# Performance work log

Hardware: AMD Instinct MI355X
Metric: run time of the kernel (lower is better)

The kernel has to match this reference:

```python
import jax, jax.numpy as jnp
import numpy as np

NUM_BINS = 4
NUM_CELLS = NUM_BINS ** 3


def _generate_grids(num_bins):
    # cell-center coordinates in the unit cube, matching generate_grids()
    c = (jnp.arange(num_bins, dtype=jnp.float32) + 1.0) / num_bins - 0.5 / num_bins
    gx, gy, gz = jnp.meshgrid(c, c, c, indexing='ij')
    return jnp.stack([gx.ravel(), gy.ravel(), gz.ravel()], axis=1)  # [C, 3]


def setup_inputs() -> dict:
    key = jax.random.key(0)
    x = jax.random.normal(key, (64, 65536, 6), dtype=jnp.float32)
    return {"input": x}


def reference(input):
    B, P, _ = input.shape
    pos = input[..., 0:3]
    ori = input[..., 3:6]

    # symmetric bounding cube: bbox_max over points and xyz dims
    bbox_max = jnp.max(jnp.abs(pos), axis=(1, 2), keepdims=True)          # [B,1,1]
    thickness = jnp.clip(2.0 * bbox_max, 1e-5, None)
    pos_in_cube = (pos + bbox_max) / thickness                            # [B,P,3] in [0,1]

    ci = jnp.clip((pos_in_cube * NUM_BINS).astype(jnp.int32), 0, NUM_BINS - 1)
    cell_idx = (ci[..., 0] * NUM_BINS + ci[..., 1]) * NUM_BINS + ci[..., 2]  # [B,P]

    seg = lambda vals, idx: jax.ops.segment_sum(vals, idx, num_segments=NUM_CELLS)

    # per-cell point counts
    freq = jax.vmap(seg)(jnp.ones((B, P), jnp.float32), cell_idx)[..., None]  # [B,C,1]
    freq_c = jnp.clip(freq, 1.0, None)
    uprefix = 1.0 / jnp.sqrt(freq_c)
    f_freq = 0.001 * freq * uprefix                                       # [B,C,1]

    # mean offset from cell centers
    grids = _generate_grids(NUM_BINS)                                     # [C,3]
    offsets = pos_in_cube - grids[cell_idx]                               # [B,P,3]
    f_mean = jax.vmap(seg)(offsets, cell_idx) * uprefix                   # [B,C,3]

    # upper-triangular orientation covariance: xx,xy,xz,yy,yz,zz
    ox, oy, oz = ori[..., 0], ori[..., 1], ori[..., 2]
    cov = jnp.stack([ox * ox, ox * oy, ox * oz, oy * oy, oy * oz, oz * oz], axis=-1)  # [B,P,6]
    f_normcov = jax.vmap(seg)(cov, cell_idx) / freq_c                     # [B,C,6]

    f_all = jnp.concatenate([f_freq, f_mean, f_normcov], axis=2).reshape(B, -1)  # [B, C*10]
    norm = jnp.linalg.norm(f_all, axis=1, keepdims=True)
    return f_all / jnp.clip(norm, 1e-12, None)
```

## Files before the change

kernel.cpp:

```cpp
#include <hip/hip_runtime.h>


#define BATCH 64
#define NPTS 65536
#define FEAT 640
#define COPIES 16
#define CSTRIDE 16
#define S_OFF 262144.0f
#define S_COV 4096.0f

__device__ __forceinline__ void bin_point(int* h, int k,
                                          float px, float py, float pz,
                                          float ox, float oy, float oz,
                                          float bmax, float inv_thick) {
    float sx = (px + bmax) * inv_thick;
    float sy = (py + bmax) * inv_thick;
    float sz = (pz + bmax) * inv_thick;
    int cx = (int)(sx * 4.0f); cx = cx < 0 ? 0 : (cx > 3 ? 3 : cx);
    int cy = (int)(sy * 4.0f); cy = cy < 0 ? 0 : (cy > 3 ? 3 : cy);
    int cz = (int)(sz * 4.0f); cz = cz < 0 ? 0 : (cz > 3 ? 3 : cz);
    int cell = (cx * 4 + cy) * 4 + cz;
    float offx = sx - (cx * 0.25f + 0.125f);
    float offy = sy - (cy * 0.25f + 0.125f);
    float offz = sz - (cz * 0.25f + 0.125f);
    int kk = k ^ (cell & 15);
    int a = cell * (10 * CSTRIDE) + kk;
    atomicAdd(&h[a + 0 * CSTRIDE], 1);
    atomicAdd(&h[a + 1 * CSTRIDE], __float2int_rn(offx * S_OFF));
    atomicAdd(&h[a + 2 * CSTRIDE], __float2int_rn(offy * S_OFF));
    atomicAdd(&h[a + 3 * CSTRIDE], __float2int_rn(offz * S_OFF));
    atomicAdd(&h[a + 4 * CSTRIDE], __float2int_rn(ox * ox * S_COV));
    atomicAdd(&h[a + 5 * CSTRIDE], __float2int_rn(ox * oy * S_COV));
    atomicAdd(&h[a + 6 * CSTRIDE], __float2int_rn(ox * oz * S_COV));
    atomicAdd(&h[a + 7 * CSTRIDE], __float2int_rn(oy * oy * S_COV));
    atomicAdd(&h[a + 8 * CSTRIDE], __float2int_rn(oy * oz * S_COV));
    atomicAdd(&h[a + 9 * CSTRIDE], __float2int_rn(oz * oz * S_COV));
}

__global__ __launch_bounds__(256) void k_bbox(const float* __restrict__ x,
                                              unsigned int* __restrict__ part,
                                              unsigned long long* __restrict__ acc) {
    int b = blockIdx.y;
    int fb = b * 16 + blockIdx.x;
    if (threadIdx.x < 40) acc[fb * 40 + threadIdx.x] = 0ULL;

    const float4* F = (const float4*)(x + (size_t)b * NPTS * 6);
    int tid = blockIdx.x * 256 + threadIdx.x;
    int tm = tid % 3;
    float m = 0.0f;
    #pragma unroll
    for (int o = 0; o < 2; ++o) {
        #pragma unroll
        for (int u = 0; u < 12; ++u) {
            int it = o * 12 + u;
            float4 v = F[tid + it * 4096];
            int mm = tm + (u % 3);
            mm = mm >= 3 ? mm - 3 : mm;
            float ax = fabsf(v.x), ay = fabsf(v.y), az = fabsf(v.z), aw = fabsf(v.w);
            float c0 = fmaxf(fmaxf(ax, ay), az);
            float c1 = fmaxf(az, aw);
            float cand = mm == 0 ? c0 : (mm == 1 ? c1 : ax);
            m = fmaxf(m, cand);
        }
    }
    for (int off = 32; off > 0; off >>= 1) m = fmaxf(m, __shfl_down(m, off, 64));
    __shared__ float s[4];
    if ((threadIdx.x & 63) == 0) s[threadIdx.x >> 6] = m;
    __syncthreads();
    if (threadIdx.x == 0) {
        m = fmaxf(fmaxf(s[0], s[1]), fmaxf(s[2], s[3]));
        part[fb] = __float_as_uint(m);
    }
}

__global__ __launch_bounds__(256) void k_bin(const float* __restrict__ x,
                                             const unsigned int* __restrict__ part,
                                             unsigned long long* __restrict__ acc) {
    __shared__ int h[FEAT * CSTRIDE];
    for (int i = threadIdx.x; i < FEAT * CSTRIDE; i += 256) h[i] = 0;
    int b = blockIdx.y;
    unsigned int um = 0u;
    #pragma unroll
    for (int p = 0; p < 16; ++p) um = um > part[b * 16 + p] ? um : part[b * 16 + p];
    float bmax = __uint_as_float(um);
    float thick = fmaxf(2.0f * bmax, 1e-5f);
    float inv_thick = 1.0f / thick;
    __syncthreads();

    const float4* base = (const float4*)(x + (size_t)b * NPTS * 6);
    int tid = blockIdx.x * 256 + threadIdx.x;
    int k = threadIdx.x & (COPIES - 1);
    #pragma unroll
    for (int it = 0; it < 8; ++it) {
        int i = tid + it * 4096;
        float4 f0 = base[3 * i + 0];
        float4 f1 = base[3 * i + 1];
        float4 f2 = base[3 * i + 2];
        bin_point(h, k, f0.x, f0.y, f0.z, f0.w, f1.x, f1.y, bmax, inv_thick);
        bin_point(h, k, f1.z, f1.w, f2.x, f2.y, f2.z, f2.w, bmax, inv_thick);
    }
    __syncthreads();
    for (int v = threadIdx.x; v < FEAT; v += 256) {
        long long sum = 0;
        #pragma unroll
        for (int c = 0; c < COPIES; ++c) sum += (long long)h[v * CSTRIDE + c];
        atomicAdd(&acc[b * FEAT + v], (unsigned long long)sum);
    }
}

__global__ __launch_bounds__(640) void k_final(const unsigned long long* __restrict__ acc,
                                               float* __restrict__ out) {
    int b = blockIdx.x;
    int t = threadIdx.x;
    int cell = t / 10, j = t - cell * 10;
    long long ni = (long long)acc[b * FEAT + cell * 10];
    long long vi = (long long)acc[b * FEAT + t];
    float n = (float)ni;
    float fc = fmaxf(n, 1.0f);
    float up = 1.0f / sqrtf(fc);
    float val;
    if (j == 0)      val = 0.001f * n * up;
    else if (j < 4)  val = ((float)vi * (1.0f / S_OFF)) * up;
    else             val = ((float)vi * (1.0f / S_COV)) / fc;

    __shared__ float red[12];
    float s = val * val;
    for (int off = 32; off > 0; off >>= 1) s += __shfl_down(s, off, 64);
    if ((t & 63) == 0) red[t >> 6] = s;
    __syncthreads();
    if (t == 0) {
        float tot = 0.0f;
        #pragma unroll
        for (int w = 0; w < 10; ++w) tot += red[w];
        red[10] = fmaxf(sqrtf(tot), 1e-12f);
    }
    __syncthreads();
    out[b * FEAT + t] = val / red[10];
}

extern "C" void kernel_launch(void* const* d_in, const int* in_sizes, int n_in,
                              void* d_out, int out_size, void* d_ws, size_t ws_size,
                              hipStream_t stream) {
    const float* x = (const float*)d_in[0];
    float* out = (float*)d_out;
    unsigned int* part = (unsigned int*)d_ws;
    unsigned long long* acc = (unsigned long long*)((char*)d_ws + 4096);

    dim3 grid(16, BATCH);
    k_bbox<<<grid, 256, 0, stream>>>(x, part, acc);
    k_bin<<<grid, 256, 0, stream>>>(x, part, acc);
    k_final<<<BATCH, 640, 0, stream>>>(acc, out);
}
```

Before: 162.2 us.

## Pack pairs of biased 32-bit accumulators into 64-bit LDS atomics

Replaces ten 32-bit shared-memory atomics per point with five 64-bit atomics, each packing two quantized feature values. Each value is biased to stay non-negative so the low half never borrows from the high half, and the bias is subtracted after reduction using the per-cell count. This halves the number of LDS atomic operations in the binning hot loop. In exchange the 64-bit atomics may be slower per operation, the cell/copy layout changes bank-conflict behaviour, and the 32-bit halves can overflow if a cell receives enough points, since each biased value can approach 2^19.

```diff
diff --git a/kernel.cpp b/kernel.cpp
--- a/kernel.cpp
+++ b/kernel.cpp
@@ -5,11 +5,12 @@
 #define NPTS 65536
 #define FEAT 640
 #define COPIES 16
-#define CSTRIDE 16
 #define S_OFF 262144.0f
 #define S_COV 4096.0f
+#define BIAS  262144
 
-__device__ __forceinline__ void bin_point(int* h, int k,
+
+__device__ __forceinline__ void bin_point(unsigned long long* h, int k,
                                           float px, float py, float pz,
                                           float ox, float oy, float oz,
                                           float bmax, float inv_thick) {
@@ -23,18 +24,22 @@
     float offx = sx - (cx * 0.25f + 0.125f);
     float offy = sy - (cy * 0.25f + 0.125f);
     float offz = sz - (cz * 0.25f + 0.125f);
+    int qx = __float2int_rn(offx * S_OFF) + BIAS;
+    int qy = __float2int_rn(offy * S_OFF) + BIAS;
+    int qz = __float2int_rn(offz * S_OFF) + BIAS;
+    int c0 = __float2int_rn(ox * ox * S_COV) + BIAS;
+    int c1 = __float2int_rn(ox * oy * S_COV) + BIAS;
+    int c2 = __float2int_rn(ox * oz * S_COV) + BIAS;
+    int c3 = __float2int_rn(oy * oy * S_COV) + BIAS;
+    int c4 = __float2int_rn(oy * oz * S_COV) + BIAS;
+    int c5 = __float2int_rn(oz * oz * S_COV) + BIAS;
     int kk = k ^ (cell & 15);
-    int a = cell * (10 * CSTRIDE) + kk;
-    atomicAdd(&h[a + 0 * CSTRIDE], 1);
-    atomicAdd(&h[a + 1 * CSTRIDE], __float2int_rn(offx * S_OFF));
-    atomicAdd(&h[a + 2 * CSTRIDE], __float2int_rn(offy * S_OFF));
-    atomicAdd(&h[a + 3 * CSTRIDE], __float2int_rn(offz * S_OFF));
-    atomicAdd(&h[a + 4 * CSTRIDE], __float2int_rn(ox * ox * S_COV));
-    atomicAdd(&h[a + 5 * CSTRIDE], __float2int_rn(ox * oy * S_COV));
-    atomicAdd(&h[a + 6 * CSTRIDE], __float2int_rn(ox * oz * S_COV));
-    atomicAdd(&h[a + 7 * CSTRIDE], __float2int_rn(oy * oy * S_COV));
-    atomicAdd(&h[a + 8 * CSTRIDE], __float2int_rn(oy * oz * S_COV));
-    atomicAdd(&h[a + 9 * CSTRIDE], __float2int_rn(oz * oz * S_COV));
+    unsigned long long* p = h + (size_t)cell * (5 * COPIES) + kk;
+    atomicAdd(p + 0 * COPIES, ((unsigned long long)(unsigned)qx << 32) | 1ULL);
+    atomicAdd(p + 1 * COPIES, ((unsigned long long)(unsigned)qz << 32) | (unsigned)qy);
+    atomicAdd(p + 2 * COPIES, ((unsigned long long)(unsigned)c1 << 32) | (unsigned)c0);
+    atomicAdd(p + 3 * COPIES, ((unsigned long long)(unsigned)c3 << 32) | (unsigned)c2);
+    atomicAdd(p + 4 * COPIES, ((unsigned long long)(unsigned)c5 << 32) | (unsigned)c4);
 }
 
 __global__ __launch_bounds__(256) void k_bbox(const float* __restrict__ x,
@@ -76,8 +81,8 @@
 __global__ __launch_bounds__(256) void k_bin(const float* __restrict__ x,
                                              const unsigned int* __restrict__ part,
                                              unsigned long long* __restrict__ acc) {
-    __shared__ int h[FEAT * CSTRIDE];
-    for (int i = threadIdx.x; i < FEAT * CSTRIDE; i += 256) h[i] = 0;
+    __shared__ unsigned long long h[64 * 5 * COPIES];
+    for (int i = threadIdx.x; i < 64 * 5 * COPIES; i += 256) h[i] = 0ULL;
     int b = blockIdx.y;
     unsigned int um = 0u;
     #pragma unroll
@@ -100,11 +105,34 @@
         bin_point(h, k, f1.z, f1.w, f2.x, f2.y, f2.z, f2.w, bmax, inv_thick);
     }
     __syncthreads();
-    for (int v = threadIdx.x; v < FEAT; v += 256) {
-        long long sum = 0;
+
+    for (int cell = threadIdx.x; cell < 64; cell += 256) {
+        unsigned long long s = 0ULL;
         #pragma unroll
-        for (int c = 0; c < COPIES; ++c) sum += (long long)h[v * CSTRIDE + c];
-        atomicAdd(&acc[b * FEAT + v], (unsigned long long)sum);
+        for (int c = 0; c < COPIES; ++c) s += h[(cell * 5 + 0) * COPIES + c];
+        h[cell * 5 * COPIES] = s;
+    }
+    __syncthreads();
+
+    for (int w = threadIdx.x; w < 320; w += 256) {
+        int cell = w / 5, f = w - cell * 5;
+        unsigned long long sc = h[cell * 5 * COPIES];
+        long long cnt = (long long)(sc & 0xffffffffULL);
+        unsigned long long s;
+        if (f == 0) {
+            s = sc;
+        } else {
+            s = 0ULL;
+            #pragma unroll
+            for (int c = 0; c < COPIES; ++c) s += h[(cell * 5 + f) * COPIES + c];
+        }
+        long long lo = (long long)(s & 0xffffffffULL);
+        long long hi = (long long)(s >> 32);
+        long long bsub = (long long)BIAS * cnt;
+        long long outLo = (f == 0) ? cnt : (lo - bsub);
+        long long outHi = hi - bsub;
+        atomicAdd(&acc[b * FEAT + cell * 10 + 2 * f + 0], (unsigned long long)outLo);
+        atomicAdd(&acc[b * FEAT + cell * 10 + 2 * f + 1], (unsigned long long)outHi);
     }
 }
 
```

After: 165.0 us. About the same (+1.7%).
